# Kernel tuning notes

Hardware: AMD Instinct MI355X
Metric: run time of the kernel (lower is better)

## Reference

```python
import jax, jax.numpy as jnp
import numpy as np

HEADS = 8
DIM_HEAD = 64
BATCH = 2  # classifier-free-guidance batch
LORA_SCALE = 1.0


def setup_inputs() -> dict:
    key = jax.random.key(0)
    ks = jax.random.split(key, 14)
    D, R = 512, 4
    BF, N = 32, 1024  # batch*frames, spatial tokens
    g = lambda k, shape, s: jax.random.normal(k, shape, dtype=jnp.float32) * s
    return {
        "hidden_states": g(ks[0], (BF, N, D), 1.0),
        "Wq": g(ks[1], (D, D), 0.02),
        "Wk": g(ks[2], (D, D), 0.02),
        "Wv": g(ks[3], (D, D), 0.02),
        "q_down": g(ks[4], (D, R), 0.25),
        "q_up": g(ks[5], (R, D), 0.02),
        "k_down": g(ks[6], (D, R), 0.25),
        "k_up": g(ks[7], (R, D), 0.02),
        "v_down": g(ks[8], (D, R), 0.25),
        "v_up": g(ks[9], (R, D), 0.02),
        "Wo": g(ks[10], (D, D), 0.02),
        "bo": jnp.zeros((D,), jnp.float32),
        "o_down": g(ks[11], (D, R), 0.25),
        "o_up": g(ks[12], (R, D), 0.02),
    }


def reference(hidden_states, Wq, Wk, Wv, q_down, q_up, k_down, k_up,
              v_down, v_up, Wo, bo, o_down, o_up):
    BF, N, C = hidden_states.shape
    F = BF // BATCH  # video_length
    inner = HEADS * DIM_HEAD

    # LoRA-augmented QKV projections (self-attention: context == hidden_states)
    q = hidden_states @ Wq + LORA_SCALE * ((hidden_states @ q_down) @ q_up)
    k = hidden_states @ Wk + LORA_SCALE * ((hidden_states @ k_down) @ k_up)
    v = hidden_states @ Wv + LORA_SCALE * ((hidden_states @ v_down) @ v_up)

    # previous-frame gather: frame f attends to frame max(f-1, 0)
    prev = jnp.concatenate([jnp.zeros((1,), jnp.int32),
                            jnp.arange(F - 1, dtype=jnp.int32)])
    k = k.reshape(BATCH, F, N, inner)[:, prev].reshape(BF, N, inner)
    v = v.reshape(BATCH, F, N, inner)[:, prev].reshape(BF, N, inner)

    def to_heads(t):  # (BF, N, inner) -> (BF*H, N, dh)
        return t.reshape(BF, N, HEADS, DIM_HEAD).transpose(0, 2, 1, 3)\
                .reshape(BF * HEADS, N, DIM_HEAD)

    qh, kh, vh = to_heads(q), to_heads(k), to_heads(v)

    scores = jnp.einsum('bid,bjd->bij', qh, kh) * (DIM_HEAD ** -0.5)
    probs = jax.nn.softmax(scores, axis=-1)
    h = jnp.einsum('bij,bjd->bid', probs, vh)

    # heads back to channel dim
    h = h.reshape(BF, HEADS, N, DIM_HEAD).transpose(0, 2, 1, 3).reshape(BF, N, inner)

    # output projection (with bias) + LoRA on the pre-projection activations
    return h @ Wo + bo + LORA_SCALE * ((h @ o_down) @ o_up)
```

## Files before the change

### kernel.cpp

```cpp
#include <hip/hip_runtime.h>
#include <hip/hip_bf16.h>
#include <math.h>

#define D512 512
#define NTOK 1024
#define QSCALE 0.1803368801111137f

typedef __attribute__((ext_vector_type(8))) short short8;
typedef __attribute__((ext_vector_type(4))) float f32x4;
typedef __attribute__((ext_vector_type(16))) float f32x16;
typedef __attribute__((ext_vector_type(4))) unsigned int u32x4;
typedef unsigned short ushort;

__device__ inline ushort f2bf(float x) {
    union { float f; unsigned u; } a; a.f = x;
    unsigned r = a.u + 0x7FFF + ((a.u >> 16) & 1);
    return (ushort)(r >> 16);
}

__device__ inline unsigned cvtpk(float a, float b) {
    unsigned r;
    asm volatile("v_cvt_pk_bf16_f32 %0, %1, %2" : "=v"(r) : "v"(a), "v"(b));
    return r;
}

__device__ inline void plswap(unsigned &a, unsigned &b) {
    asm volatile("v_permlane32_swap_b32 %0, %1" : "+v"(a), "+v"(b));
}

#define GLL16(src, dst) __builtin_amdgcn_global_load_lds( \
    (const __attribute__((address_space(1))) unsigned int*)(src), \
    (__attribute__((address_space(3))) unsigned int*)(dst), 16, 0, 0)

__global__ __launch_bounds__(256) void cvt_bf16(
    const float* __restrict__ in, ushort* __restrict__ out)
{
    const int idx = blockIdx.x * 256 + threadIdx.x;
    float4 a = ((const float4*)in)[idx * 2];
    float4 b = ((const float4*)in)[idx * 2 + 1];
    short8 s;
    s[0] = f2bf(a.x); s[1] = f2bf(a.y); s[2] = f2bf(a.z); s[3] = f2bf(a.w);
    s[4] = f2bf(b.x); s[5] = f2bf(b.y); s[6] = f2bf(b.z); s[7] = f2bf(b.w);
    *(short8*)&out[(size_t)idx * 8] = s;
}

__global__ __launch_bounds__(256) void fold_weights_T(
    const float* __restrict__ Wq, const float* __restrict__ Wk,
    const float* __restrict__ Wv, const float* __restrict__ Wo,
    const float* __restrict__ qd, const float* __restrict__ qu,
    const float* __restrict__ kd, const float* __restrict__ ku,
    const float* __restrict__ vd, const float* __restrict__ vu,
    const float* __restrict__ od, const float* __restrict__ ou,
    ushort* __restrict__ out)
{
    const int which = blockIdx.y;
    const float *W, *dn, *up;
    if (which == 0)      { W = Wq; dn = qd; up = qu; }
    else if (which == 1) { W = Wk; dn = kd; up = ku; }
    else if (which == 2) { W = Wv; dn = vd; up = vu; }
    else                 { W = Wo; dn = od; up = ou; }

    const int td = (blockIdx.x >> 3) * 64;
    const int te = (blockIdx.x & 7) * 64;
    __shared__ float T[64][65];
    const int r4 = threadIdx.x >> 6;
    const int c  = threadIdx.x & 63;

    #pragma unroll
    for (int i = 0; i < 16; ++i) {
        int row = i * 4 + r4;
        T[row][c] = W[(size_t)(td + row) * 512 + te + c];
    }
    __syncthreads();
    #pragma unroll
    for (int i = 0; i < 16; ++i) {
        int e = te + i * 4 + r4;
        int d = td + c;
        float s = T[c][i * 4 + r4];
        #pragma unroll
        for (int r = 0; r < 4; ++r) s += dn[d * 4 + r] * up[r * 512 + e];
        out[(size_t)which * 262144 + (size_t)e * 512 + d] = f2bf(s);
    }
}

#define SWZT(r, c) ((((r) * 128) + (c)) ^ (((r) & 7) << 3))

template<int QKV>
__global__ __launch_bounds__(256) void gemm_mfma(
    const ushort* __restrict__ A, const ushort* __restrict__ BT,
    const float* __restrict__ bias, float* __restrict__ Co,
    ushort* __restrict__ qb, ushort* __restrict__ kb, ushort* __restrict__ vtb)
{
    __shared__ ushort smem[16384];

    const int tid = threadIdx.x;
    const int w = tid >> 6, l = tid & 63;
    const int l15 = l & 15, l4 = l >> 4;

    const int wg = blockIdx.x;
    const int rxcd = wg & 7, t = wg >> 3;
    const int NX = QKV ? 12 : 4;
    const int xb = t % NX, yh = t / NX;
    const int yb = (yh << 3) | rxcd;
    const int m0 = yb * 128;
    const int n0 = xb * 128;

    const int srow = l >> 2;
    const int scol = (l & 3) * 8;
    const ushort* Asrc = A  + (size_t)(m0 + w * 32 + srow) * 512 + scol;
    const ushort* Bsrc = BT + (size_t)(n0 + w * 32 + srow) * 512 + scol;

    const int wm = (w >> 1) * 64, wn = (w & 1) * 64;

    f32x4 acc[4][4] = {};

    {
        ushort* AsW = smem + w * 1024;
        ushort* BsW = smem + 4096 + w * 1024;
        GLL16(Asrc, AsW);            GLL16(Asrc + 16 * 512, AsW + 512);
        GLL16(Bsrc, BsW);            GLL16(Bsrc + 16 * 512, BsW + 512);
    }
    __syncthreads();

    int cur = 0;
    for (int k0 = 0; k0 < 512; k0 += 32) {
        if (k0 < 480) {
            ushort* AsW = smem + (cur ^ 1) * 8192 + w * 1024;
            ushort* BsW = smem + (cur ^ 1) * 8192 + 4096 + w * 1024;
            GLL16(Asrc + k0 + 32, AsW);
            GLL16(Asrc + k0 + 32 + 16 * 512, AsW + 512);
            GLL16(Bsrc + k0 + 32, BsW);
            GLL16(Bsrc + k0 + 32 + 16 * 512, BsW + 512);
        }
        const ushort* As = smem + cur * 8192;
        const ushort* Bs = smem + cur * 8192 + 4096;

        short8 bfr[4];
        #pragma unroll
        for (int ni = 0; ni < 4; ++ni)
            bfr[ni] = *(const short8*)&Bs[(wn + ni * 16 + l15) * 32 + l4 * 8];
        __builtin_amdgcn_s_setprio(1);
        #pragma unroll
        for (int mi = 0; mi < 4; ++mi) {
            short8 af = *(const short8*)&As[(wm + mi * 16 + l15) * 32 + l4 * 8];
            #pragma unroll
            for (int ni = 0; ni < 4; ++ni)
                acc[mi][ni] = __builtin_amdgcn_mfma_f32_16x16x32_bf16(
                    af, bfr[ni], acc[mi][ni], 0, 0, 0);
        }
        __builtin_amdgcn_s_setprio(0);
        __syncthreads();
        cur ^= 1;
    }

    if (QKV) {
        const int which = xb >> 2;
        if (which < 2) {
            const float sc = which ? 1.0f : QSCALE;
            ushort* dst = which ? kb : qb;
            const int headbase = (n0 & 511) >> 6;
            #pragma unroll
            for (int h = 0; h < 2; ++h) {
                if (wm == h * 64) {
                    #pragma unroll
                    for (int mi = 0; mi < 4; ++mi)
                        #pragma unroll
                        for (int j = 0; j < 4; ++j) {
                            const int r = mi * 16 + l4 * 4 + j;
                            #pragma unroll
                            for (int ni = 0; ni < 4; ++ni) {
                                const int c = wn + ni * 16 + l15;
                                smem[SWZT(r, c)] = f2bf(acc[mi][ni][j] * sc);
                            }
                        }
                }
                __syncthreads();
                const int rr2 = tid >> 4;
                const int cc2 = (tid & 15) * 8;
                const int chunk = cc2 >> 6;
                const int d0 = cc2 & 63;
                #pragma unroll
                for (int s = 0; s < 4; ++s) {
                    const int r = s * 16 + rr2;
                    const int token = m0 + h * 64 + r;
                    const size_t off = (((size_t)(token >> 10) * 8 + headbase + chunk)
                                        * NTOK + (token & 1023)) * 64 + d0;
                    *(u32x4*)&dst[off] = *(const u32x4*)&smem[SWZT(r, cc2)];
                }
                if (h == 0) __syncthreads();
            }
        } else {
            #pragma unroll
            for (int mi = 0; mi < 4; ++mi) {
                const int rowb = m0 + wm + mi * 16 + l4 * 4;
                const int nn = rowb & 1023;
                const int bf8 = (rowb >> 10) * 8;
                #pragma unroll
                for (int ni = 0; ni < 4; ++ni) {
                    const int col = (n0 & 511) + wn + ni * 16 + l15;
                    const int d = col & 63, head = (col >> 6) & 7;
                    unsigned w0 = cvtpk(acc[mi][ni][0], acc[mi][ni][1]);
                    unsigned w1 = cvtpk(acc[mi][ni][2], acc[mi][ni][3]);
                    *(unsigned long long*)&vtb[((size_t)(bf8 + head) * 64 + d) * NTOK + nn] =
                        (unsigned long long)w0 | ((unsigned long long)w1 << 32);
                }
            }
        }
    } else {
        float bvals[4];
        #pragma unroll
        for (int ni = 0; ni < 4; ++ni)
            bvals[ni] = bias[n0 + wn + ni * 16 + l15];
        #pragma unroll
        for (int mi = 0; mi < 4; ++mi)
            #pragma unroll
            for (int j = 0; j < 4; ++j) {
                const int row = m0 + wm + mi * 16 + l4 * 4 + j;
                #pragma unroll
                for (int ni = 0; ni < 4; ++ni) {
                    const int col = n0 + wn + ni * 16 + l15;
                    Co[(size_t)row * 512 + col] = acc[mi][ni][j] + bvals[ni];
                }
            }
    }
}

#define SWZ(r, c)  ((((r) * 64) + (c)) ^ (((r) & 7) << 3))
#define VSWZ(r, c) ((((r) * 32) + (c)) ^ ((((r) >> 1) & 3) << 3))

#define SOFTPACK32(sv, lsum, pa) { \
    unsigned pk[4][2]; \
    float ls = 0.f; \
    _Pragma("unroll") \
    for (int rq = 0; rq < 4; ++rq) { \
        float p0 = __builtin_amdgcn_exp2f(sv[4 * rq + 0]); \
        float p1 = __builtin_amdgcn_exp2f(sv[4 * rq + 1]); \
        float p2 = __builtin_amdgcn_exp2f(sv[4 * rq + 2]); \
        float p3 = __builtin_amdgcn_exp2f(sv[4 * rq + 3]); \
        ls += (p0 + p1) + (p2 + p3); \
        pk[rq][0] = cvtpk(p0, p1); \
        pk[rq][1] = cvtpk(p2, p3); \
    } \
    lsum += ls; \
    _Pragma("unroll") \
    for (int kc = 0; kc < 2; ++kc) { \
        unsigned a0 = pk[2 * kc][0], b0 = pk[2 * kc + 1][0]; \
        unsigned a1 = pk[2 * kc][1], b1 = pk[2 * kc + 1][1]; \
        plswap(a0, b0); \
        plswap(a1, b1); \
        pa[kc].u[0] = a0; pa[kc].u[1] = a1; \
        pa[kc].u[2] = b0; pa[kc].u[3] = b1; \
    } }

__global__ __launch_bounds__(64, 2) void attn_wave(
    const ushort* __restrict__ qb, const ushort* __restrict__ kb,
    const ushort* __restrict__ vtb, ushort* __restrict__ hb)
{
    __shared__ ushort smem[8192];

    const int l = threadIdx.x;
    const int l31 = l & 31, hi = l >> 5;

    const int wg = blockIdx.x;
    const int rxcd = wg & 7, t = wg >> 3;
    const int qt = t & 15;
    const int bh = ((t >> 4) << 3) | rxcd;

    const size_t qbase = (size_t)bh * 65536;
    const int src_bh = ((bh >> 3) & 15) ? bh - 8 : bh;
    const size_t kvbase = (size_t)src_bh * 65536;

    const int qrowA = qt * 64 + l31;
    const ushort* qpA = qb + qbase + (size_t)qrowA * 64 + hi * 8;
    const ushort* qpB = qpA + 32 * 64;
    short8 qfA[4], qfB[4];
    #pragma unroll
    for (int dq = 0; dq < 4; ++dq) {
        qfA[dq] = *(const short8*)(qpA + dq * 16);
        qfB[dq] = *(const short8*)(qpB + dq * 16);
    }

    f32x16 accA0 = {}, accA1 = {}, accB0 = {}, accB1 = {};
    float lsumA = 0.f, lsumB = 0.f;

    const int klr = l >> 3, klc = l & 7;
    const int kck = (klc ^ klr) * 8;
    const int vro = l >> 2, vch = l & 3;

#define STAGE32(ktv, b) { \
    ushort* KD = smem + (b) * 4096; \
    ushort* VD = smem + (b) * 4096 + 2048; \
    const ushort* ksrc = kb + kvbase + (size_t)((ktv) * 32) * 64; \
    _Pragma("unroll") \
    for (int j = 0; j < 4; ++j) \
        GLL16(ksrc + (size_t)(j * 8 + klr) * 64 + kck, KD + j * 512); \
    _Pragma("unroll") \
    for (int j = 0; j < 4; ++j) { \
        const int rv = j * 16 + vro; \
        GLL16(vtb + kvbase + (size_t)rv * 1024 + (ktv) * 32 \
              + ((vch ^ ((rv >> 1) & 3)) * 8), VD + j * 512); \
    } }

    STAGE32(0, 0);

    int cur = 0;
    for (int kt = 0; kt < 32; ++kt) {
        asm volatile("s_waitcnt vmcnt(0)" ::: "memory");
        __builtin_amdgcn_sched_barrier(0);
        if (kt < 31) STAGE32(kt + 1, cur ^ 1);
        const ushort* Ks = smem + cur * 4096;
        const ushort* Vt = smem + cur * 4096 + 2048;

        f32x16 svA = {}, svB = {};
        __builtin_amdgcn_s_setprio(1);
        #pragma unroll
        for (int dq = 0; dq < 4; ++dq) {
            short8 kf = *(const short8*)&Ks[SWZ(l31, dq * 16 + hi * 8)];
            svA = __builtin_amdgcn_mfma_f32_32x32x16_bf16(kf, qfA[dq], svA, 0, 0, 0);
            svB = __builtin_amdgcn_mfma_f32_32x32x16_bf16(kf, qfB[dq], svB, 0, 0, 0);
        }
        __builtin_amdgcn_s_setprio(0);

        union { u32x4 u; short8 s; } paA[2], paB[2];
        SOFTPACK32(svA, lsumA, paA);
        SOFTPACK32(svB, lsumB, paB);

        __builtin_amdgcn_s_setprio(1);
        #pragma unroll
        for (int kc = 0; kc < 2; ++kc) {
            short8 vf0 = *(const short8*)&Vt[VSWZ(l31,      kc * 16 + hi * 8)];
            short8 vf1 = *(const short8*)&Vt[VSWZ(32 + l31, kc * 16 + hi * 8)];
            accA0 = __builtin_amdgcn_mfma_f32_32x32x16_bf16(vf0, paA[kc].s, accA0, 0, 0, 0);
            accA1 = __builtin_amdgcn_mfma_f32_32x32x16_bf16(vf1, paA[kc].s, accA1, 0, 0, 0);
            accB0 = __builtin_amdgcn_mfma_f32_32x32x16_bf16(vf0, paB[kc].s, accB0, 0, 0, 0);
            accB1 = __builtin_amdgcn_mfma_f32_32x32x16_bf16(vf1, paB[kc].s, accB1, 0, 0, 0);
        }
        __builtin_amdgcn_s_setprio(0);
        cur ^= 1;
    }
#undef STAGE32

    {
        unsigned au = __float_as_uint(lsumA), bu = au;
        plswap(au, bu);
        lsumA = __uint_as_float(au) + __uint_as_float(bu);
        unsigned cu2 = __float_as_uint(lsumB), du = cu2;
        plswap(cu2, du);
        lsumB = __uint_as_float(cu2) + __uint_as_float(du);
    }

    ushort* tw = smem;
    const int q2 = l >> 1, ch = (l & 1) * 32;
    {
        const float inv = 1.f / lsumA;
        #pragma unroll
        for (int r = 0; r < 16; ++r) {
            const int d = (r & 3) + 8 * (r >> 2) + 4 * hi;
            tw[SWZ(l31, d)]      = f2bf(accA0[r] * inv);
            tw[SWZ(l31, 32 + d)] = f2bf(accA1[r] * inv);
        }
        const int hrow = qt * 64 + q2;
        ushort* gdst = hb + ((size_t)(bh >> 3) * NTOK + hrow) * D512 + (bh & 7) * 64 + ch;
        #pragma unroll
        for (int c = 0; c < 4; ++c)
            *(u32x4*)(gdst + c * 8) = *(const u32x4*)&tw[SWZ(q2, ch + c * 8)];
    }
    __builtin_amdgcn_s_waitcnt(0);
    {
        const float inv = 1.f / lsumB;
        #pragma unroll
        for (int r = 0; r < 16; ++r) {
            const int d = (r & 3) + 8 * (r >> 2) + 4 * hi;
            tw[SWZ(l31, d)]      = f2bf(accB0[r] * inv);
            tw[SWZ(l31, 32 + d)] = f2bf(accB1[r] * inv);
        }
        const int hrow = qt * 64 + 32 + q2;
        ushort* gdst = hb + ((size_t)(bh >> 3) * NTOK + hrow) * D512 + (bh & 7) * 64 + ch;
        #pragma unroll
        for (int c = 0; c < 4; ++c)
            *(u32x4*)(gdst + c * 8) = *(const u32x4*)&tw[SWZ(q2, ch + c * 8)];
    }
}

extern "C" void kernel_launch(void* const* d_in, const int* in_sizes, int n_in,
                              void* d_out, int out_size, void* d_ws, size_t ws_size,
                              hipStream_t stream)
{
    const float* hs = (const float*)d_in[0];
    const float* Wq = (const float*)d_in[1];
    const float* Wk = (const float*)d_in[2];
    const float* Wv = (const float*)d_in[3];
    const float* qd = (const float*)d_in[4];
    const float* qu = (const float*)d_in[5];
    const float* kd = (const float*)d_in[6];
    const float* ku = (const float*)d_in[7];
    const float* vd = (const float*)d_in[8];
    const float* vu = (const float*)d_in[9];
    const float* Wo = (const float*)d_in[10];
    const float* bo = (const float*)d_in[11];
    const float* od = (const float*)d_in[12];
    const float* ou = (const float*)d_in[13];

    ushort* wsb = (ushort*)d_ws;
    ushort* WT  = wsb;
    ushort* hsb = wsb + 1048576;
    ushort* qb  = hsb + 16777216;
    ushort* kb  = qb  + 16777216;
    ushort* vtb = kb  + 16777216;
    ushort* hbb = vtb + 16777216;

    float* out = (float*)d_out;

    cvt_bf16<<<dim3(8192), 256, 0, stream>>>(hs, hsb);
    fold_weights_T<<<dim3(64, 4), 256, 0, stream>>>(
        Wq, Wk, Wv, Wo, qd, qu, kd, ku, vd, vu, od, ou, WT);

    gemm_mfma<1><<<dim3(3072), 256, 0, stream>>>(
        hsb, WT, nullptr, nullptr, qb, kb, vtb);

    attn_wave<<<dim3(4096), 64, 0, stream>>>(qb, kb, vtb, hbb);

    gemm_mfma<0><<<dim3(1024), 256, 0, stream>>>(
        hbb, WT + 786432, bo, out, nullptr, nullptr, nullptr);
}
```

Baseline: 218.3 us.

## Load K/V MFMA fragments directly from global memory, dropping LDS staging

The attention kernel no longer double-buffers K and V^T tiles into LDS through direct global-to-LDS loads. Each lane now reads its MFMA operand fragments straight from global memory every key tile, and LDS is kept only as a small transpose buffer for the output. This removes the LDS round trip and the vmcnt waits, and shrinks shared memory so more waves can be resident. In exchange the loads are no longer prefetched a tile ahead, so global and L2 latency is exposed unless the compiler or occupancy hides it. The launch-bounds occupancy hint is also dropped.

```diff
diff --git a/kernel.cpp b/kernel.cpp
--- a/kernel.cpp
+++ b/kernel.cpp
@@ -226,7 +226,6 @@
 }
 
 #define SWZ(r, c)  ((((r) * 64) + (c)) ^ (((r) & 7) << 3))
-#define VSWZ(r, c) ((((r) * 32) + (c)) ^ ((((r) >> 1) & 3) << 3))
 
 #define SOFTPACK32(sv, lsum, pa) { \
     unsigned pk[4][2]; \
@@ -252,11 +251,11 @@
         pa[kc].u[2] = b0; pa[kc].u[3] = b1; \
     } }
 
-__global__ __launch_bounds__(64, 2) void attn_wave(
+__global__ __launch_bounds__(64) void attn_frag(
     const ushort* __restrict__ qb, const ushort* __restrict__ kb,
     const ushort* __restrict__ vtb, ushort* __restrict__ hb)
 {
-    __shared__ ushort smem[8192];
+    __shared__ ushort Tr[2048];
 
     const int l = threadIdx.x;
     const int l31 = l & 31, hi = l >> 5;
@@ -280,45 +279,33 @@
         qfB[dq] = *(const short8*)(qpB + dq * 16);
     }
 
+    const ushort* kbl  = kb  + kvbase + (size_t)l31 * 64 + hi * 8;
+    const ushort* vbl0 = vtb + kvbase + (size_t)l31 * 1024 + hi * 8;
+    const ushort* vbl1 = vbl0 + 32 * 1024;
+
     f32x16 accA0 = {}, accA1 = {}, accB0 = {}, accB1 = {};
     float lsumA = 0.f, lsumB = 0.f;
 
-    const int klr = l >> 3, klc = l & 7;
-    const int kck = (klc ^ klr) * 8;
-    const int vro = l >> 2, vch = l & 3;
-
-#define STAGE32(ktv, b) { \
-    ushort* KD = smem + (b) * 4096; \
-    ushort* VD = smem + (b) * 4096 + 2048; \
-    const ushort* ksrc = kb + kvbase + (size_t)((ktv) * 32) * 64; \
-    _Pragma("unroll") \
-    for (int j = 0; j < 4; ++j) \
-        GLL16(ksrc + (size_t)(j * 8 + klr) * 64 + kck, KD + j * 512); \
-    _Pragma("unroll") \
-    for (int j = 0; j < 4; ++j) { \
-        const int rv = j * 16 + vro; \
-        GLL16(vtb + kvbase + (size_t)rv * 1024 + (ktv) * 32 \
-              + ((vch ^ ((rv >> 1) & 3)) * 8), VD + j * 512); \
-    } }
-
-    STAGE32(0, 0);
-
-    int cur = 0;
     for (int kt = 0; kt < 32; ++kt) {
-        asm volatile("s_waitcnt vmcnt(0)" ::: "memory");
-        __builtin_amdgcn_sched_barrier(0);
-        if (kt < 31) STAGE32(kt + 1, cur ^ 1);
-        const ushort* Ks = smem + cur * 4096;
-        const ushort* Vt = smem + cur * 4096 + 2048;
+        short8 kf0 = *(const short8*)(kbl + kt * 2048);
+        short8 kf1 = *(const short8*)(kbl + kt * 2048 + 16);
+        short8 kf2 = *(const short8*)(kbl + kt * 2048 + 32);
+        short8 kf3 = *(const short8*)(kbl + kt * 2048 + 48);
+        short8 vfa0 = *(const short8*)(vbl0 + kt * 32);
+        short8 vfa1 = *(const short8*)(vbl0 + kt * 32 + 16);
+        short8 vfb0 = *(const short8*)(vbl1 + kt * 32);
+        short8 vfb1 = *(const short8*)(vbl1 + kt * 32 + 16);
 
         f32x16 svA = {}, svB = {};
         __builtin_amdgcn_s_setprio(1);
-        #pragma unroll
-        for (int dq = 0; dq < 4; ++dq) {
-            short8 kf = *(const short8*)&Ks[SWZ(l31, dq * 16 + hi * 8)];
-            svA = __builtin_amdgcn_mfma_f32_32x32x16_bf16(kf, qfA[dq], svA, 0, 0, 0);
-            svB = __builtin_amdgcn_mfma_f32_32x32x16_bf16(kf, qfB[dq], svB, 0, 0, 0);
-        }
+        svA = __builtin_amdgcn_mfma_f32_32x32x16_bf16(kf0, qfA[0], svA, 0, 0, 0);
+        svB = __builtin_amdgcn_mfma_f32_32x32x16_bf16(kf0, qfB[0], svB, 0, 0, 0);
+        svA = __builtin_amdgcn_mfma_f32_32x32x16_bf16(kf1, qfA[1], svA, 0, 0, 0);
+        svB = __builtin_amdgcn_mfma_f32_32x32x16_bf16(kf1, qfB[1], svB, 0, 0, 0);
+        svA = __builtin_amdgcn_mfma_f32_32x32x16_bf16(kf2, qfA[2], svA, 0, 0, 0);
+        svB = __builtin_amdgcn_mfma_f32_32x32x16_bf16(kf2, qfB[2], svB, 0, 0, 0);
+        svA = __builtin_amdgcn_mfma_f32_32x32x16_bf16(kf3, qfA[3], svA, 0, 0, 0);
+        svB = __builtin_amdgcn_mfma_f32_32x32x16_bf16(kf3, qfB[3], svB, 0, 0, 0);
         __builtin_amdgcn_s_setprio(0);
 
         union { u32x4 u; short8 s; } paA[2], paB[2];
@@ -326,19 +313,16 @@
         SOFTPACK32(svB, lsumB, paB);
 
         __builtin_amdgcn_s_setprio(1);
-        #pragma unroll
-        for (int kc = 0; kc < 2; ++kc) {
-            short8 vf0 = *(const short8*)&Vt[VSWZ(l31,      kc * 16 + hi * 8)];
-            short8 vf1 = *(const short8*)&Vt[VSWZ(32 + l31, kc * 16 + hi * 8)];
-            accA0 = __builtin_amdgcn_mfma_f32_32x32x16_bf16(vf0, paA[kc].s, accA0, 0, 0, 0);
-            accA1 = __builtin_amdgcn_mfma_f32_32x32x16_bf16(vf1, paA[kc].s, accA1, 0, 0, 0);
-            accB0 = __builtin_amdgcn_mfma_f32_32x32x16_bf16(vf0, paB[kc].s, accB0, 0, 0, 0);
-            accB1 = __builtin_amdgcn_mfma_f32_32x32x16_bf16(vf1, paB[kc].s, accB1, 0, 0, 0);
-        }
+        accA0 = __builtin_amdgcn_mfma_f32_32x32x16_bf16(vfa0, paA[0].s, accA0, 0, 0, 0);
+        accA1 = __builtin_amdgcn_mfma_f32_32x32x16_bf16(vfb0, paA[0].s, accA1, 0, 0, 0);
+        accB0 = __builtin_amdgcn_mfma_f32_32x32x16_bf16(vfa0, paB[0].s, accB0, 0, 0, 0);
+        accB1 = __builtin_amdgcn_mfma_f32_32x32x16_bf16(vfb0, paB[0].s, accB1, 0, 0, 0);
+        accA0 = __builtin_amdgcn_mfma_f32_32x32x16_bf16(vfa1, paA[1].s, accA0, 0, 0, 0);
+        accA1 = __builtin_amdgcn_mfma_f32_32x32x16_bf16(vfb1, paA[1].s, accA1, 0, 0, 0);
+        accB0 = __builtin_amdgcn_mfma_f32_32x32x16_bf16(vfa1, paB[1].s, accB0, 0, 0, 0);
+        accB1 = __builtin_amdgcn_mfma_f32_32x32x16_bf16(vfb1, paB[1].s, accB1, 0, 0, 0);
         __builtin_amdgcn_s_setprio(0);
-        cur ^= 1;
-    }
-#undef STAGE32
+    }
 
     {
         unsigned au = __float_as_uint(lsumA), bu = au;
@@ -349,7 +333,7 @@
         lsumB = __uint_as_float(cu2) + __uint_as_float(du);
     }
 
-    ushort* tw = smem;
+    ushort* tw = Tr;
     const int q2 = l >> 1, ch = (l & 1) * 32;
     {
         const float inv = 1.f / lsumA;
@@ -418,7 +402,7 @@
     gemm_mfma<1><<<dim3(3072), 256, 0, stream>>>(
         hsb, WT, nullptr, nullptr, qb, kb, vtb);
 
-    attn_wave<<<dim3(4096), 64, 0, stream>>>(qb, kb, vtb, hbb);
+    attn_frag<<<dim3(4096), 64, 0, stream>>>(qb, kb, vtb, hbb);
 
     gemm_mfma<0><<<dim3(1024), 256, 0, stream>>>(
         hbb, WT + 786432, bo, out, nullptr, nullptr, nullptr);
```

Measured after the change: 255.6 us. +17.1%, slower.
